# Kernel optimization log

Hardware: AMD Instinct MI355X
Metric: run time of the kernel (lower is better)

Reference implementation:

```python
import jax, jax.numpy as jnp
import numpy as np

B, S, D_IN, D_OUT = 4, 2048, 1024, 1024


def setup_inputs() -> dict:
    key = jax.random.key(0)
    k1, k2, k3, k4 = jax.random.split(key, 4)
    scale = 1.0 / np.sqrt(D_IN)
    return {
        "x": jax.random.normal(k1, (B, S, D_IN), dtype=jnp.float32),
        "W_q": jax.random.normal(k2, (D_OUT, D_IN), dtype=jnp.float32) * scale,
        "W_k": jax.random.normal(k3, (D_OUT, D_IN), dtype=jnp.float32) * scale,
        "W_v": jax.random.normal(k4, (D_OUT, D_IN), dtype=jnp.float32) * scale,
    }


def reference(x, W_q, W_k, W_v):
    # torch nn.Linear: y = x @ W.T (bias=False)
    q = jnp.einsum("bsd,od->bso", x, W_q)
    k = jnp.einsum("bsd,od->bso", x, W_k)
    v = jnp.einsum("bsd,od->bso", x, W_v)
    s = q.shape[1]
    scores = jnp.einsum("bqo,bko->bqk", q, k)  # [B, S, S]
    causal = jnp.triu(jnp.ones((s, s), dtype=bool), k=1)
    scores = jnp.where(causal, -jnp.inf, scores)
    inv_sqrt_d = 1.0 / jnp.sqrt(jnp.asarray(q.shape[-1], scores.dtype))
    attn = jax.nn.softmax(scores * inv_sqrt_d, axis=-1)
    # dropout p=0.0 -> identity (deterministic reference)
    return jnp.einsum("bqk,bko->bqo", attn, v)
```

## Files before the change

kernel.cpp:

```cpp
#include <hip/hip_runtime.h>

typedef unsigned short u16;
typedef unsigned int u32;
typedef __bf16 bf16x8 __attribute__((ext_vector_type(8)));
typedef float f32x4 __attribute__((ext_vector_type(4)));

#define AS1 __attribute__((address_space(1)))
#define AS3 __attribute__((address_space(3)))

__device__ inline u16 f2bf(float f) {
  union { float f; unsigned u; } a; a.f = f;
  unsigned u = a.u;
  return (u16)((u + 0x7fffu + ((u >> 16) & 1u)) >> 16);
}
__device__ inline float bf2f(u16 h) {
  union { unsigned u; float f; } a; a.u = ((u32)h) << 16; return a.f;
}

__global__ __launch_bounds__(256) void cvt_all_kernel(
    const float* __restrict__ x, const float* __restrict__ wq,
    const float* __restrict__ wk, const float* __restrict__ wv,
    u16* __restrict__ xb, u16* __restrict__ wqb,
    u16* __restrict__ wkb, u16* __restrict__ wvb) {
  int bid = blockIdx.x;
  const float* in; u16* out;
  if (bid < 8192) { in = x; out = xb; }
  else if (bid < 9216) { in = wq; out = wqb; bid -= 8192; }
  else if (bid < 10240) { in = wk; out = wkb; bid -= 9216; }
  else { in = wv; out = wvb; bid -= 10240; }
  size_t i = ((size_t)bid * 256 + threadIdx.x) * 4;
  float4 v = *(const float4*)(in + i);
  ushort4 o;
  o.x = f2bf(v.x); o.y = f2bf(v.y); o.z = f2bf(v.z); o.w = f2bf(v.w);
  *(ushort4*)(out + i) = o;
}

template <typename CT>
__device__ __forceinline__ void gemm_core3(
    u16* __restrict__ lds,
    const u16* __restrict__ A, const u16* __restrict__ B, CT* __restrict__ C,
    int nt, int lda, int ldb, int ldc, int m0, int n0) {
  const int tid = threadIdx.x;
  const int ln = tid & 63, wv = tid >> 6;
  const int wr = wv >> 2, wc = wv & 3;

  auto sweep = [&](const u16* src, int ld, int t, int s, int base) {
    const int c = s * 512 + tid;
    const int row = c >> 3, slot = c & 7;
    const int col = (slot ^ (row & 7)) * 8;
    __builtin_amdgcn_global_load_lds(
        (const AS1 void*)(src + (size_t)row * ld + (size_t)t * 64 + col),
        (AS3 void*)(&lds[base + c * 8]), 16, 0, 0);
  };

  f32x4 acc[8][4] = {};

#pragma unroll
  for (int s = 0; s < 4; ++s) sweep(B, ldb, 0, s, 49152);
#pragma unroll
  for (int s = 0; s < 4; ++s) sweep(A, lda, 0, s, 0);
  if (nt > 1) {
#pragma unroll
    for (int s = 0; s < 4; ++s) sweep(B, ldb, 1, s, 65536);
#pragma unroll
    for (int s = 0; s < 4; ++s) sweep(A, lda, 1, s, 16384);
    asm volatile("s_waitcnt vmcnt(8)" ::: "memory");
  } else {
    asm volatile("s_waitcnt vmcnt(0)" ::: "memory");
  }
  __builtin_amdgcn_s_barrier();

  for (int t = 0; t < nt; ++t) {
    const u16* La = &lds[(t % 3) * 16384];
    const u16* Lb = &lds[49152 + (t & 1) * 16384];
    const int an = ((t + 2) % 3) * 16384;
    const int bn = 49152 + (t & 1) * 16384;
    bf16x8 bfr[4][2];
#pragma unroll
    for (int q = 0; q < 4; ++q) {
      if (q == 0) {
        __builtin_amdgcn_sched_barrier(0);
#pragma unroll
        for (int ni = 0; ni < 4; ++ni)
#pragma unroll
          for (int ks = 0; ks < 2; ++ks) {
            const int row = wc * 64 + ni * 16 + (ln & 15);
            const int kc = ks * 4 + (ln >> 4);
            bfr[ni][ks] = *(const bf16x8*)&Lb[row * 64 + ((kc ^ (row & 7)) << 3)];
          }
      }
      bf16x8 afr[2][2];
#pragma unroll
      for (int mi = 0; mi < 2; ++mi)
#pragma unroll
        for (int ks = 0; ks < 2; ++ks) {
          const int row = wr * 128 + (q * 2 + mi) * 16 + (ln & 15);
          const int kc = ks * 4 + (ln >> 4);
          afr[mi][ks] = *(const bf16x8*)&La[row * 64 + ((kc ^ (row & 7)) << 3)];
        }
      if (t + 2 < nt) {
        if (q == 0)      { sweep(A, lda, t + 2, 0, an); sweep(A, lda, t + 2, 1, an); }
        else if (q == 1) { sweep(A, lda, t + 2, 2, an); sweep(A, lda, t + 2, 3, an); }
        else if (q == 2) { sweep(B, ldb, t + 2, 0, bn); sweep(B, ldb, t + 2, 1, bn); }
        else             { sweep(B, ldb, t + 2, 2, bn); sweep(B, ldb, t + 2, 3, bn); }
      }

      __builtin_amdgcn_s_barrier();
      __builtin_amdgcn_s_setprio(1);
#pragma unroll
      for (int mi = 0; mi < 2; ++mi)
#pragma unroll
        for (int ni = 0; ni < 4; ++ni)
#pragma unroll
          for (int ks = 0; ks < 2; ++ks)
            acc[q * 2 + mi][ni] = __builtin_amdgcn_mfma_f32_16x16x32_bf16(
                afr[mi][ks], bfr[ni][ks], acc[q * 2 + mi][ni], 0, 0, 0);
      __builtin_amdgcn_s_setprio(0);
      if (q == 3) {
        if (t + 2 < nt)      asm volatile("s_waitcnt vmcnt(8)" ::: "memory");
        else if (t + 1 < nt) asm volatile("s_waitcnt vmcnt(0)" ::: "memory");
      }
      __builtin_amdgcn_s_barrier();
    }
  }

#pragma unroll
  for (int mi = 0; mi < 8; ++mi) {
    const int rbase = m0 + wr * 128 + mi * 16 + (ln >> 4) * 4;
#pragma unroll
    for (int ni = 0; ni < 4; ++ni) {
      const int col = n0 + wc * 64 + ni * 16 + (ln & 15);
#pragma unroll
      for (int r = 0; r < 4; ++r) {
        const float v = acc[mi][ni][r];
        CT* ptr = &C[(size_t)(rbase + r) * ldc + col];
        if constexpr (sizeof(CT) == 4) *(float*)ptr = v;
        else                           *ptr = f2bf(v);
      }
    }
  }
}

__global__ __launch_bounds__(512, 2) void proj_qk_kernel(
    const u16* __restrict__ xb, const u16* __restrict__ wqb,
    const u16* __restrict__ wkb, u16* __restrict__ Qb, u16* __restrict__ Kb) {
  __shared__ __align__(16) u16 lds[81920];
  const int bid = blockIdx.x;
  const int w = bid >> 7, r = bid & 127;
  const int rb = r >> 2, n0 = (r & 3) * 256;
  const u16* B = w ? wkb : wqb;
  u16* C = w ? Kb : Qb;
  gemm_core3<u16>(lds, xb + (size_t)rb * 256 * 1024, B + (size_t)n0 * 1024,
                  C, 16, 1024, 1024, 1024, rb * 256, n0);
}

__global__ __launch_bounds__(512, 2) void qktvt_kernel(
    const u16* __restrict__ Qb, const u16* __restrict__ Kb, u16* __restrict__ Sb16,
    const u16* __restrict__ wvb, const u16* __restrict__ xb, u16* __restrict__ VTb) {
  __shared__ __align__(16) u16 lds[81920];
  const int bid = blockIdx.x;
  const int item = (bid & 7) * 32 + (bid >> 3);
  if (item < 144) {
    const int z = item / 36, xt = item % 36;
    int m = 0;
    while ((m + 1) * (m + 2) / 2 <= xt) ++m;
    const int n = xt - m * (m + 1) / 2;
    gemm_core3<u16>(lds,
        Qb + ((size_t)z * 2048 + m * 256) * 1024,
        Kb + ((size_t)z * 2048 + n * 256) * 1024,
        Sb16 + (size_t)z * 2048 * 2048,
        16, 1024, 1024, 2048, m * 256, n * 256);
  } else {
    const int j = item - 144;
    const int z = j / 28, r2 = j % 28, d = r2 / 7, kb = r2 % 7;
    gemm_core3<u16>(lds, wvb + (size_t)d * 256 * 1024,
                    xb + (size_t)z * 2048 * 1024 + (size_t)kb * 256 * 1024,
                    VTb + (size_t)z * 1024 * 2048,
                    16, 1024, 1024, 2048, d * 256, kb * 256);
  }
}

__global__ __launch_bounds__(512, 2) void smvt_kernel(
    u16* __restrict__ Sb16, float* __restrict__ R,
    const u16* __restrict__ wvb, const u16* __restrict__ xb) {
  __shared__ __align__(16) u16 lds[81920];
  const int bid = blockIdx.x;
  const int tid = threadIdx.x;
  if (bid < 64) {
    const int z = bid >> 4, r = bid & 15;
    const int d = r >> 2, h = r & 3;
    const u16* A = wvb + (size_t)d * 256 * 1024 + h * 256;
    const u16* B = xb + ((size_t)z * 2048 + 1792) * 1024 + h * 256;
    float* C = R + (size_t)z * 2097152 + (d * 4 + h) * 65536;
    gemm_core3<float>(lds, A, B, C, 4, 1024, 1024, 256, 0, 0);
    return;
  }
  const int j = bid - 64;
  const int m = 7 - (j >> 6), z = (j >> 4) & 3, s = j & 15;
  const int iters = (m + 2) >> 1;
  const int wvid = tid >> 6, lane = tid & 63;
  u16* S0 = Sb16 + (size_t)z * 2048 * 2048;
  for (int rr = wvid; rr < 16; rr += 8) {
    const int r = m * 256 + s * 16 + rr;
    u16* row = S0 + (size_t)r * 2048;
    float vals[4][8];
    float mx = -3.4e38f;
#pragma unroll
    for (int it2 = 0; it2 < 4; ++it2)
      if (it2 < iters) {
        const int idx8 = it2 * 512 + lane * 8;
        uint4 w = *(const uint4*)(row + idx8);
        const u32 ws[4] = {w.x, w.y, w.z, w.w};
#pragma unroll
        for (int e = 0; e < 8; ++e) {
          const u16 hb = (u16)(ws[e >> 1] >> ((e & 1) * 16));
          const float xv = bf2f(hb) * 0.03125f;
          vals[it2][e] = (idx8 + e <= r) ? xv : -3.4e38f;
          mx = fmaxf(mx, vals[it2][e]);
        }
      }
#pragma unroll
    for (int o = 32; o; o >>= 1) mx = fmaxf(mx, __shfl_xor(mx, o, 64));
    float sum = 0.f;
#pragma unroll
    for (int it2 = 0; it2 < 4; ++it2)
      if (it2 < iters) {
#pragma unroll
        for (int e = 0; e < 8; ++e) {
          const float pp = __expf(vals[it2][e] - mx);
          vals[it2][e] = pp;
          sum += pp;
        }
      }
#pragma unroll
    for (int o = 32; o; o >>= 1) sum += __shfl_xor(sum, o, 64);
    const float rcp = 1.f / sum;
#pragma unroll
    for (int it2 = 0; it2 < 4; ++it2)
      if (it2 < iters) {
        const int idx8 = it2 * 512 + lane * 8;
        uint4 w;
        u32 wo[4];
#pragma unroll
        for (int e2 = 0; e2 < 4; ++e2) {
          const u16 lo = f2bf(vals[it2][e2 * 2] * rcp);
          const u16 hi = f2bf(vals[it2][e2 * 2 + 1] * rcp);
          wo[e2] = (u32)lo | ((u32)hi << 16);
        }
        w.x = wo[0]; w.y = wo[1]; w.z = wo[2]; w.w = wo[3];
        *(uint4*)(row + idx8) = w;
      }
  }
}

__global__ __launch_bounds__(256) void vtfix_kernel(const float* __restrict__ R,
                                                    u16* __restrict__ VTb) {
  const int bid = blockIdx.x;
  const int z = bid >> 3, q = bid & 7;
  const int d = q >> 1, rh = q & 1;
  const float* P0 = R + (size_t)z * 2097152 + (d * 4 + 0) * 65536;
  const float* P1 = P0 + 65536;
  const float* P2 = P0 + 131072;
  const float* P3 = P0 + 196608;
  for (int k = threadIdx.x; k < 128 * 64; k += 256) {
    const int dp = rh * 128 + (k >> 6), c4 = (k & 63) * 4;
    const size_t off = (size_t)dp * 256 + c4;
    float4 a = *(const float4*)(P0 + off);
    float4 b = *(const float4*)(P1 + off);
    float4 c = *(const float4*)(P2 + off);
    float4 e = *(const float4*)(P3 + off);
    ushort4 o;
    o.x = f2bf(a.x + b.x + c.x + e.x); o.y = f2bf(a.y + b.y + c.y + e.y);
    o.z = f2bf(a.z + b.z + c.z + e.z); o.w = f2bf(a.w + b.w + c.w + e.w);
    *(ushort4*)(VTb + (size_t)z * 1024 * 2048 + (size_t)(d * 256 + dp) * 2048 +
                1792 + c4) = o;
  }
}

__constant__ signed char CPM[16] = {5,5,7,7,7,6,4,4,6,6,3,3,1,2,2,0};
__constant__ signed char CPK[16] = {0,12,0,11,22,0,0,10,10,19,0,8,0,0,6,0};
__constant__ signed char CPN[16] = {12,12,11,11,10,10,10,10,9,9,8,8,8,6,6,4};
__constant__ signed char CPS[16] = {0,1,0,1,2,0,0,1,1,2,0,1,0,0,1,0};

__global__ __launch_bounds__(512, 2) void pv_kernel(
    const u16* __restrict__ P, const u16* __restrict__ VTb,
    float* __restrict__ out, char* __restrict__ R) {
  __shared__ __align__(16) u16 lds[81920];
  const int cls = blockIdx.x, n = blockIdx.y;
  const size_t z = blockIdx.z;
  const int m = CPM[cls], k0 = CPK[cls], ntc = CPN[cls], sl = CPS[cls];
  const u16* Ap = P + z * 2048 * 2048 + (size_t)m * 256 * 2048 + (size_t)k0 * 64;
  const u16* Bp = VTb + z * 1024 * 2048 + (size_t)n * 256 * 2048 + (size_t)k0 * 64;
  if (sl == 0) {
    gemm_core3<float>(lds, Ap, Bp, out + z * 2048 * 1024, ntc,
                      2048, 2048, 1024, m * 256, n * 256);
  } else if (sl == 1) {
    u16* s1 = (u16*)(R + z * (8ul << 20) + (4ul << 20)) - (size_t)512 * 1024;
    gemm_core3<u16>(lds, Ap, Bp, s1, ntc, 2048, 2048, 1024, m * 256, n * 256);
  } else {
    u16* s2 = (u16*)(R + z * (8ul << 20) + (7ul << 20)) - (size_t)1536 * 1024;
    gemm_core3<u16>(lds, Ap, Bp, s2, ntc, 2048, 2048, 1024, m * 256, n * 256);
  }
}

__global__ __launch_bounds__(256) void reduce_kernel(float* __restrict__ out,
                                                     const char* __restrict__ R) {
  const int j = blockIdx.x;
  const int m = 2 + (j >> 5), z = (j >> 3) & 3, s = j & 7;
  float* ob = out + (size_t)z * 2048 * 1024;
  const u16* s1 = (const u16*)(R + (size_t)z * (8ul << 20) + (4ul << 20));
  const u16* s2 = (const u16*)(R + (size_t)z * (8ul << 20) + (7ul << 20));
  const int r0 = m * 256 + s * 32;
  for (int k = threadIdx.x; k < 32 * 256; k += 256) {
    const int rr = r0 + (k >> 8), cc = k & 255;
    float4 o = ((float4*)(ob + (size_t)rr * 1024))[cc];
    ushort4 a = ((const ushort4*)(s1 + (size_t)(rr - 512) * 1024))[cc];
    o.x += bf2f(a.x); o.y += bf2f(a.y); o.z += bf2f(a.z); o.w += bf2f(a.w);
    if (m >= 6) {
      ushort4 b = ((const ushort4*)(s2 + (size_t)(rr - 1536) * 1024))[cc];
      o.x += bf2f(b.x); o.y += bf2f(b.y); o.z += bf2f(b.z); o.w += bf2f(b.w);
    }
    ((float4*)(ob + (size_t)rr * 1024))[cc] = o;
  }
}

extern "C" void kernel_launch(void* const* d_in, const int* in_sizes, int n_in,
                              void* d_out, int out_size, void* d_ws, size_t ws_size,
                              hipStream_t stream) {
  const float* x  = (const float*)d_in[0];
  const float* Wq = (const float*)d_in[1];
  const float* Wk = (const float*)d_in[2];
  const float* Wv = (const float*)d_in[3];
  float* out = (float*)d_out;

  char* ws = (char*)d_ws;
  u16* xb   = (u16*)(ws);
  u16* wqb  = (u16*)(ws + (16ul << 20));
  u16* wkb  = (u16*)(ws + (18ul << 20));
  u16* wvb  = (u16*)(ws + (20ul << 20));
  u16* Qb   = (u16*)(ws + (22ul << 20));
  u16* Kb   = (u16*)(ws + (38ul << 20));
  u16* VTb  = (u16*)(ws + (54ul << 20));
  u16* Sb16 = (u16*)(ws + (70ul << 20));
  char* R   = ws + (102ul << 20);

  cvt_all_kernel<<<11264, 256, 0, stream>>>(x, Wq, Wk, Wv, xb, wqb, wkb, wvb);

  proj_qk_kernel<<<256, 512, 0, stream>>>(xb, wqb, wkb, Qb, Kb);

  qktvt_kernel<<<256, 512, 0, stream>>>(Qb, Kb, Sb16, wvb, xb, VTb);

  smvt_kernel<<<576, 512, 0, stream>>>(Sb16, (float*)R, wvb, xb);

  vtfix_kernel<<<32, 256, 0, stream>>>((const float*)R, VTb);

  pv_kernel<<<dim3(16, 4, 4), 512, 0, stream>>>(Sb16, VTb, out, R);

  reduce_kernel<<<192, 256, 0, stream>>>(out, R);
}
```

Baseline: 162.6 us.

## Use 128x128 tiles for QK^T and V^T GEMMs, drop split-K V^T fixup

Adds a 128x128-tile GEMM core with a smaller LDS footprint and occupancy 4, and uses it for the causal QK^T tiles and the full V^T projection in one 1056-block launch. The separate split-K V^T path for the last 256 columns and its fp32 reduction kernel are removed, so softmax runs alone in its own kernel. This is meant to improve load balance and wave fill across CUs and to cut two launches and the partial-sum traffic. The cost is lower arithmetic intensity per tile, which means more global and LDS traffic per FLOP.

```diff
diff --git a/kernel.cpp b/kernel.cpp
--- a/kernel.cpp
+++ b/kernel.cpp
@@ -141,6 +141,105 @@
   }
 }
 
+template <typename CT>
+__device__ __forceinline__ void gemm_core128(
+    u16* __restrict__ lds,
+    const u16* __restrict__ A, const u16* __restrict__ B, CT* __restrict__ C,
+    int nt, int lda, int ldb, int ldc, int m0, int n0) {
+  const int tid = threadIdx.x;
+  const int ln = tid & 63, wv = tid >> 6;
+  const int wr = wv >> 1, wc = wv & 1;
+
+  auto sweep = [&](const u16* src, int ld, int t, int s, int base) {
+    const int c = s * 512 + tid;
+    const int row = c >> 3, slot = c & 7;
+    const int col = (slot ^ (row & 7)) * 8;
+    __builtin_amdgcn_global_load_lds(
+        (const AS1 void*)(src + (size_t)row * ld + (size_t)t * 64 + col),
+        (AS3 void*)(&lds[base + c * 8]), 16, 0, 0);
+  };
+
+  f32x4 acc[2][4] = {};
+
+  sweep(B, ldb, 0, 0, 24576); sweep(B, ldb, 0, 1, 24576);
+  sweep(A, lda, 0, 0, 0);     sweep(A, lda, 0, 1, 0);
+  if (nt > 1) {
+    sweep(B, ldb, 1, 0, 32768); sweep(B, ldb, 1, 1, 32768);
+    sweep(A, lda, 1, 0, 8192);  sweep(A, lda, 1, 1, 8192);
+    asm volatile("s_waitcnt vmcnt(4)" ::: "memory");
+  } else {
+    asm volatile("s_waitcnt vmcnt(0)" ::: "memory");
+  }
+  __builtin_amdgcn_s_barrier();
+
+  for (int t = 0; t < nt; ++t) {
+    const u16* La = &lds[(t % 3) * 8192];
+    const u16* Lb = &lds[24576 + (t & 1) * 8192];
+    const int an = ((t + 2) % 3) * 8192;
+    const int bn = 24576 + (t & 1) * 8192;
+
+    __builtin_amdgcn_sched_barrier(0);
+    bf16x8 bfr[4][2], afr[2][2];
+#pragma unroll
+    for (int ni = 0; ni < 4; ++ni)
+#pragma unroll
+      for (int ks = 0; ks < 2; ++ks) {
+        const int row = wc * 64 + ni * 16 + (ln & 15);
+        const int kc = ks * 4 + (ln >> 4);
+        bfr[ni][ks] = *(const bf16x8*)&Lb[row * 64 + ((kc ^ (row & 7)) << 3)];
+      }
+#pragma unroll
+    for (int mi = 0; mi < 2; ++mi)
+#pragma unroll
+      for (int ks = 0; ks < 2; ++ks) {
+        const int row = wr * 32 + mi * 16 + (ln & 15);
+        const int kc = ks * 4 + (ln >> 4);
+        afr[mi][ks] = *(const bf16x8*)&La[row * 64 + ((kc ^ (row & 7)) << 3)];
+      }
+    if (t + 2 < nt) { sweep(A, lda, t + 2, 0, an); sweep(A, lda, t + 2, 1, an); }
+    __builtin_amdgcn_s_barrier();
+    __builtin_amdgcn_s_setprio(1);
+#pragma unroll
+    for (int ni = 0; ni < 4; ++ni)
+#pragma unroll
+      for (int ks = 0; ks < 2; ++ks)
+        acc[0][ni] = __builtin_amdgcn_mfma_f32_16x16x32_bf16(
+            afr[0][ks], bfr[ni][ks], acc[0][ni], 0, 0, 0);
+    __builtin_amdgcn_s_setprio(0);
+    __builtin_amdgcn_s_barrier();
+
+    if (t + 2 < nt) { sweep(B, ldb, t + 2, 0, bn); sweep(B, ldb, t + 2, 1, bn); }
+    __builtin_amdgcn_s_barrier();
+    __builtin_amdgcn_s_setprio(1);
+#pragma unroll
+    for (int ni = 0; ni < 4; ++ni)
+#pragma unroll
+      for (int ks = 0; ks < 2; ++ks)
+        acc[1][ni] = __builtin_amdgcn_mfma_f32_16x16x32_bf16(
+            afr[1][ks], bfr[ni][ks], acc[1][ni], 0, 0, 0);
+    __builtin_amdgcn_s_setprio(0);
+    if (t + 2 < nt)      asm volatile("s_waitcnt vmcnt(4)" ::: "memory");
+    else if (t + 1 < nt) asm volatile("s_waitcnt vmcnt(0)" ::: "memory");
+    __builtin_amdgcn_s_barrier();
+  }
+
+#pragma unroll
+  for (int mi = 0; mi < 2; ++mi) {
+    const int rbase = m0 + wr * 32 + mi * 16 + (ln >> 4) * 4;
+#pragma unroll
+    for (int ni = 0; ni < 4; ++ni) {
+      const int col = n0 + wc * 64 + ni * 16 + (ln & 15);
+#pragma unroll
+      for (int r = 0; r < 4; ++r) {
+        const float v = acc[mi][ni][r];
+        CT* ptr = &C[(size_t)(rbase + r) * ldc + col];
+        if constexpr (sizeof(CT) == 4) *(float*)ptr = v;
+        else                           *ptr = f2bf(v);
+      }
+    }
+  }
+}
+
 __global__ __launch_bounds__(512, 2) void proj_qk_kernel(
     const u16* __restrict__ xb, const u16* __restrict__ wqb,
     const u16* __restrict__ wkb, u16* __restrict__ Qb, u16* __restrict__ Kb) {
@@ -154,50 +253,38 @@
                   C, 16, 1024, 1024, 1024, rb * 256, n0);
 }
 
-__global__ __launch_bounds__(512, 2) void qktvt_kernel(
+__global__ __launch_bounds__(512, 4) void qktvt128_kernel(
     const u16* __restrict__ Qb, const u16* __restrict__ Kb, u16* __restrict__ Sb16,
     const u16* __restrict__ wvb, const u16* __restrict__ xb, u16* __restrict__ VTb) {
-  __shared__ __align__(16) u16 lds[81920];
+  __shared__ __align__(16) u16 lds[40960];
   const int bid = blockIdx.x;
-  const int item = (bid & 7) * 32 + (bid >> 3);
-  if (item < 144) {
-    const int z = item / 36, xt = item % 36;
-    int m = 0;
-    while ((m + 1) * (m + 2) / 2 <= xt) ++m;
-    const int n = xt - m * (m + 1) / 2;
-    gemm_core3<u16>(lds,
-        Qb + ((size_t)z * 2048 + m * 256) * 1024,
-        Kb + ((size_t)z * 2048 + n * 256) * 1024,
+  const int item = (bid & 7) * 132 + (bid >> 3);
+  if (item < 544) {
+    const int z = item / 136, ti = item % 136;
+    int i = 0;
+    while ((i + 1) * (i + 2) / 2 <= ti) ++i;
+    const int j = ti - i * (i + 1) / 2;
+    gemm_core128<u16>(lds,
+        Qb + ((size_t)z * 2048 + i * 128) * 1024,
+        Kb + ((size_t)z * 2048 + j * 128) * 1024,
         Sb16 + (size_t)z * 2048 * 2048,
-        16, 1024, 1024, 2048, m * 256, n * 256);
+        16, 1024, 1024, 2048, i * 128, j * 128);
   } else {
-    const int j = item - 144;
-    const int z = j / 28, r2 = j % 28, d = r2 / 7, kb = r2 % 7;
-    gemm_core3<u16>(lds, wvb + (size_t)d * 256 * 1024,
-                    xb + (size_t)z * 2048 * 1024 + (size_t)kb * 256 * 1024,
-                    VTb + (size_t)z * 1024 * 2048,
-                    16, 1024, 1024, 2048, d * 256, kb * 256);
-  }
-}
-
-__global__ __launch_bounds__(512, 2) void smvt_kernel(
-    u16* __restrict__ Sb16, float* __restrict__ R,
-    const u16* __restrict__ wvb, const u16* __restrict__ xb) {
-  __shared__ __align__(16) u16 lds[81920];
-  const int bid = blockIdx.x;
-  const int tid = threadIdx.x;
-  if (bid < 64) {
-    const int z = bid >> 4, r = bid & 15;
-    const int d = r >> 2, h = r & 3;
-    const u16* A = wvb + (size_t)d * 256 * 1024 + h * 256;
-    const u16* B = xb + ((size_t)z * 2048 + 1792) * 1024 + h * 256;
-    float* C = R + (size_t)z * 2097152 + (d * 4 + h) * 65536;
-    gemm_core3<float>(lds, A, B, C, 4, 1024, 1024, 256, 0, 0);
-    return;
-  }
-  const int j = bid - 64;
+    const int v = item - 544;
+    const int z = v >> 7, r = v & 127;
+    const int d = r >> 4, k = r & 15;
+    gemm_core128<u16>(lds, wvb + (size_t)d * 128 * 1024,
+                      xb + ((size_t)z * 2048 + k * 128) * 1024,
+                      VTb + (size_t)z * 1024 * 2048,
+                      16, 1024, 1024, 2048, d * 128, k * 128);
+  }
+}
+
+__global__ __launch_bounds__(512) void sm_kernel(u16* __restrict__ Sb16) {
+  const int j = blockIdx.x;
   const int m = 7 - (j >> 6), z = (j >> 4) & 3, s = j & 15;
   const int iters = (m + 2) >> 1;
+  const int tid = threadIdx.x;
   const int wvid = tid >> 6, lane = tid & 63;
   u16* S0 = Sb16 + (size_t)z * 2048 * 2048;
   for (int rr = wvid; rr < 16; rr += 8) {
@@ -250,30 +337,6 @@
         w.x = wo[0]; w.y = wo[1]; w.z = wo[2]; w.w = wo[3];
         *(uint4*)(row + idx8) = w;
       }
-  }
-}
-
-__global__ __launch_bounds__(256) void vtfix_kernel(const float* __restrict__ R,
-                                                    u16* __restrict__ VTb) {
-  const int bid = blockIdx.x;
-  const int z = bid >> 3, q = bid & 7;
-  const int d = q >> 1, rh = q & 1;
-  const float* P0 = R + (size_t)z * 2097152 + (d * 4 + 0) * 65536;
-  const float* P1 = P0 + 65536;
-  const float* P2 = P0 + 131072;
-  const float* P3 = P0 + 196608;
-  for (int k = threadIdx.x; k < 128 * 64; k += 256) {
-    const int dp = rh * 128 + (k >> 6), c4 = (k & 63) * 4;
-    const size_t off = (size_t)dp * 256 + c4;
-    float4 a = *(const float4*)(P0 + off);
-    float4 b = *(const float4*)(P1 + off);
-    float4 c = *(const float4*)(P2 + off);
-    float4 e = *(const float4*)(P3 + off);
-    ushort4 o;
-    o.x = f2bf(a.x + b.x + c.x + e.x); o.y = f2bf(a.y + b.y + c.y + e.y);
-    o.z = f2bf(a.z + b.z + c.z + e.z); o.w = f2bf(a.w + b.w + c.w + e.w);
-    *(ushort4*)(VTb + (size_t)z * 1024 * 2048 + (size_t)(d * 256 + dp) * 2048 +
-                1792 + c4) = o;
   }
 }
 
@@ -348,11 +411,9 @@
 
   proj_qk_kernel<<<256, 512, 0, stream>>>(xb, wqb, wkb, Qb, Kb);
 
-  qktvt_kernel<<<256, 512, 0, stream>>>(Qb, Kb, Sb16, wvb, xb, VTb);
-
-  smvt_kernel<<<576, 512, 0, stream>>>(Sb16, (float*)R, wvb, xb);
-
-  vtfix_kernel<<<32, 256, 0, stream>>>((const float*)R, VTb);
+  qktvt128_kernel<<<1056, 512, 0, stream>>>(Qb, Kb, Sb16, wvb, xb, VTb);
+
+  sm_kernel<<<512, 512, 0, stream>>>(Sb16);
 
   pv_kernel<<<dim3(16, 4, 4), 512, 0, stream>>>(Sb16, VTb, out, R);
 
```

New measurement: 158.5 us, median of 2. -2.5%, faster.
